# Optimization experiments

Measured on AMD Instinct MI355X. Metric: run time of the kernel, lower is better.

The kernel has to match this reference:

```python
import jax, jax.numpy as jnp
import numpy as np

D, P, R, F = 512, 64, 32, 256  # directions, points per ray, rank, virtual subcarriers


def setup_inputs() -> dict:
    key = jax.random.key(0)
    ks = jax.random.split(key, 6)
    return {
        "att_re": jax.random.normal(ks[0], (D, P, R), dtype=jnp.float32),
        "att_im": jax.random.normal(ks[1], (D, P, R), dtype=jnp.float32),
        "rad_re": jax.random.normal(ks[2], (D, P, R), dtype=jnp.float32),
        "rad_im": jax.random.normal(ks[3], (D, P, R), dtype=jnp.float32),
        "freq_re": jax.random.normal(ks[4], (F, R), dtype=jnp.float32),
        "freq_im": jax.random.normal(ks[5], (F, R), dtype=jnp.float32),
        "max_ray_length": 200,
    }


def reference(att_re, att_im, rad_re, rad_im, freq_re, freq_im, max_ray_length):
    att = (att_re + 1j * att_im).astype(jnp.complex64)   # (D,P,R)
    rad = (rad_re + 1j * rad_im).astype(jnp.complex64)   # (D,P,R)
    fv = (freq_re + 1j * freq_im).astype(jnp.complex64)  # (F,R)

    num_points = att.shape[1]
    num_dirs = att.shape[0]
    delta_t = jnp.asarray(max_ray_length / num_points, dtype=jnp.float32)

    # prefix-sum of conjugated attenuation along the ray (u_hat_rho)
    u_hat_rho = jnp.cumsum(att.conj() * delta_t, axis=1)  # (D,P,R)

    # Project each rank-R vector onto each frequency basis vector.
    # The original's v_outer / v_outer_outer einsums factor exactly into these dot products.
    a_proj = jnp.einsum('dpr,fr->dpf', att.conj(), fv)        # (D,P,F)
    r_proj = jnp.einsum('dpr,fr->dpf', rad.conj(), fv)        # (D,P,F)
    u_proj = jnp.einsum('dpr,fr->dpf', u_hat_rho.conj(), fv)  # (D,P,F)

    # first-order: sum over all points; second-order: points k >= 1 only
    first = jnp.sum(r_proj * a_proj, axis=(0, 1))                                   # (F,)
    second = jnp.sum(r_proj[:, 1:] * a_proj[:, 1:] * u_proj[:, 1:], axis=(0, 1))    # (F,)

    csi = (first + second) * delta_t / num_dirs  # (F,) complex64
    return csi
```

## Files before the change

kernel.cpp:

```cpp
#include <hip/hip_runtime.h>

#define ND 512
#define NP 64
#define NR 32
#define NF 256
#define RS 40

typedef __attribute__((ext_vector_type(8))) short bf16x8;
typedef __attribute__((ext_vector_type(4))) float f32x4;
typedef __attribute__((ext_vector_type(4))) unsigned int uint4v;

__device__ inline unsigned short f2bf(float x) {
    unsigned u = __builtin_bit_cast(unsigned, x);
    u += 0x7FFFu + ((u >> 16) & 1u);
    return (unsigned short)(u >> 16);
}
__device__ inline unsigned pack2(float a, float b) {
    return (unsigned)f2bf(a) | ((unsigned)f2bf(b) << 16);
}
__device__ inline bf16x8 neg8(bf16x8 v) {
    uint4v u = __builtin_bit_cast(uint4v, v);
    u ^= (uint4v){0x80008000u, 0x80008000u, 0x80008000u, 0x80008000u};
    return __builtin_bit_cast(bf16x8, u);
}

__global__ __launch_bounds__(256) void lrrt_bprep_kernel(
    const float* __restrict__ fre, const float* __restrict__ fim,
    unsigned short* __restrict__ ws)
{
    const int tid = blockIdx.x * 256 + threadIdx.x;
    const int plane = tid >> 11;
    const int i4 = (tid & 2047) * 4;
    const float* src = plane ? fim : fre;
    const float4 x = *(const float4*)(src + i4);
    *(uint2*)(ws + plane * (NF * NR) + i4) = make_uint2(pack2(x.x, x.y), pack2(x.z, x.w));
}

__global__ __launch_bounds__(256, 4) void lrrt_main_kernel(
    const float* __restrict__ att_re, const float* __restrict__ att_im,
    const float* __restrict__ rad_re, const float* __restrict__ rad_im,
    const unsigned short* __restrict__ wsB, const int* __restrict__ mrl,
    float* __restrict__ out)
{
    __shared__ __align__(16) unsigned short s_a[6][NP * RS];
    __shared__ float s_tot[256];
    __shared__ float s_red[4][128][2];

    const int t = threadIdx.x;
    const int h = blockIdx.x & 1;
    const int d = blockIdx.x >> 1;
    const size_t base = (size_t)d * (NP * NR);
    const int lane = t & 63, wv = t >> 6, kg = lane >> 4, m_lo = lane & 15;
    const float dt = (float)(*mrl) / (float)NP;

#pragma unroll
    for (int half = 0; half < 2; ++half) {
        const int w = t + half * 256;
        const int p = w >> 3;
        const int c = (w & 7) * 4;
        const size_t g = base + (size_t)p * NR + c;
        const int lo = p * RS + c;
        float4 x;
        x = *(const float4*)(att_re + g);
        *(uint2*)&s_a[0][lo] = make_uint2(pack2(x.x, x.y), pack2(x.z, x.w));
        x = *(const float4*)(att_im + g);
        *(uint2*)&s_a[1][lo] = make_uint2(pack2(x.x, x.y), pack2(x.z, x.w));
        x = *(const float4*)(rad_re + g);
        *(uint2*)&s_a[2][lo] = make_uint2(pack2(x.x, x.y), pack2(x.z, x.w));
        x = *(const float4*)(rad_im + g);
        *(uint2*)&s_a[3][lo] = make_uint2(pack2(x.x, x.y), pack2(x.z, x.w));
    }

    const int cs_r = t & 31, cs_reim = (t >> 5) & 1, cs_seg = t >> 6;
    float vals[16];
    {
        const float* src = cs_reim ? att_im : att_re;
        float run = 0.f;
#pragma unroll
        for (int i = 0; i < 16; ++i) {
            run += src[base + (size_t)(cs_seg * 16 + i) * NR + cs_r];
            vals[i] = run;
        }
        s_tot[t] = run;
    }
    __syncthreads();

    {
        float off = 0.f;
#pragma unroll
        for (int s = 0; s < 3; ++s)
            if (s < cs_seg) off += s_tot[s * 64 + cs_reim * 32 + cs_r];
        const float sc = cs_reim ? -dt : dt;
        unsigned short* dst = s_a[4 + cs_reim];
#pragma unroll
        for (int i = 0; i < 16; ++i) {
            const int p = cs_seg * 16 + i;
            dst[p * RS + cs_r] = (p == 0) ? (unsigned short)0
                                          : f2bf(sc * (vals[i] + off));
        }
    }
    __syncthreads();

    const int aoff = (wv * 16 + m_lo) * RS + 8 * kg;
    const bf16x8 a_r = *(const bf16x8*)&s_a[0][aoff];
    const bf16x8 a_i = *(const bf16x8*)&s_a[1][aoff];
    const bf16x8 r_r = *(const bf16x8*)&s_a[2][aoff];
    const bf16x8 r_i = *(const bf16x8*)&s_a[3][aoff];
    const bf16x8 c_r = *(const bf16x8*)&s_a[4][aoff];
    const bf16x8 c_i = *(const bf16x8*)&s_a[5][aoff];

    const f32x4 zero = {0.f, 0.f, 0.f, 0.f};

#pragma unroll 1
    for (int q = 0; q < 8; ++q) {
        const int f = 16 * (8 * h + q) + m_lo;
        const size_t boff = (size_t)f * NR + 8 * kg;
        const bf16x8 vr = *(const bf16x8*)(wsB + boff);
        const bf16x8 vi = *(const bf16x8*)(wsB + NF * NR + boff);
        const bf16x8 vn = neg8(vr);

        f32x4 Are = __builtin_amdgcn_mfma_f32_16x16x32_bf16(a_r, vr, zero, 0, 0, 0);
        f32x4 Aim = __builtin_amdgcn_mfma_f32_16x16x32_bf16(a_r, vi, zero, 0, 0, 0);
        f32x4 Bre = __builtin_amdgcn_mfma_f32_16x16x32_bf16(r_r, vr, zero, 0, 0, 0);
        f32x4 Bim = __builtin_amdgcn_mfma_f32_16x16x32_bf16(r_r, vi, zero, 0, 0, 0);
        f32x4 Ure = __builtin_amdgcn_mfma_f32_16x16x32_bf16(c_r, vr, zero, 0, 0, 0);
        f32x4 Uim = __builtin_amdgcn_mfma_f32_16x16x32_bf16(c_r, vi, zero, 0, 0, 0);
        Are = __builtin_amdgcn_mfma_f32_16x16x32_bf16(a_i, vi, Are, 0, 0, 0);
        Aim = __builtin_amdgcn_mfma_f32_16x16x32_bf16(a_i, vn, Aim, 0, 0, 0);
        Bre = __builtin_amdgcn_mfma_f32_16x16x32_bf16(r_i, vi, Bre, 0, 0, 0);
        Bim = __builtin_amdgcn_mfma_f32_16x16x32_bf16(r_i, vn, Bim, 0, 0, 0);
        Ure = __builtin_amdgcn_mfma_f32_16x16x32_bf16(c_i, vi, Ure, 0, 0, 0);
        Uim = __builtin_amdgcn_mfma_f32_16x16x32_bf16(c_i, vn, Uim, 0, 0, 0);

        float sr = 0.f, si = 0.f;
#pragma unroll
        for (int i = 0; i < 4; ++i) {
            const float qre = Bre[i] * Are[i] - Bim[i] * Aim[i];
            const float qim = Bre[i] * Aim[i] + Bim[i] * Are[i];
            const float cre = 1.0f + Ure[i];
            const float cim = Uim[i];
            sr = fmaf(qre, cre, fmaf(-qim, cim, sr));
            si = fmaf(qim, cre, fmaf(qre, cim, si));
        }
        sr += __shfl_xor(sr, 16, 64); si += __shfl_xor(si, 16, 64);
        sr += __shfl_xor(sr, 32, 64); si += __shfl_xor(si, 32, 64);
        if (lane < 16) {
            s_red[wv][16 * q + lane][0] = sr;
            s_red[wv][16 * q + lane][1] = si;
        }
    }
    __syncthreads();

    const float scale = dt / (float)ND;
    {
        const int lf = t >> 1, comp = t & 1;
        const float v = s_red[0][lf][comp] + s_red[1][lf][comp]
                      + s_red[2][lf][comp] + s_red[3][lf][comp];
        atomicAdd(&out[comp * NF + h * 128 + lf], v * scale);
    }
}

extern "C" void kernel_launch(void* const* d_in, const int* in_sizes, int n_in,
                              void* d_out, int out_size, void* d_ws, size_t ws_size,
                              hipStream_t stream) {
    const float* att_re = (const float*)d_in[0];
    const float* att_im = (const float*)d_in[1];
    const float* rad_re = (const float*)d_in[2];
    const float* rad_im = (const float*)d_in[3];
    const float* freq_re = (const float*)d_in[4];
    const float* freq_im = (const float*)d_in[5];
    const int* mrl = (const int*)d_in[6];
    float* out = (float*)d_out;
    unsigned short* ws = (unsigned short*)d_ws;

    hipMemsetAsync(d_out, 0, (size_t)out_size * sizeof(float), stream);

    lrrt_bprep_kernel<<<16, 256, 0, stream>>>(freq_re, freq_im, ws);
    lrrt_main_kernel<<<2 * ND, 256, 0, stream>>>(
        att_re, att_im, rad_re, rad_im, ws, mrl, out);
}
```

Measured before the change: 96.74 us.

## Move attenuation prefix-sum into prep kernel and load MFMA operands directly from global

The cumulative sum of attenuation along each ray is now computed once in the prep kernel and stored as bf16 in workspace. Previously both halves of each direction repeated it in the main kernel. The main kernel drops its shared-memory staging and both block barriers, loading and converting its MFMA A operands straight from global memory into registers. The cost is an extra workspace round trip and a serial 64-step scan per thread in the prep kernel, which has only 128 blocks and may be latency bound.

```diff
diff --git a/kernel.cpp b/kernel.cpp
--- a/kernel.cpp
+++ b/kernel.cpp
@@ -4,7 +4,10 @@
 #define NP 64
 #define NR 32
 #define NF 256
-#define RS 40
+
+#define PLANE (ND * NP * NR)
+#define B0 (2 * PLANE)
+#define B1 (2 * PLANE + NF * NR)
 
 typedef __attribute__((ext_vector_type(8))) short bf16x8;
 typedef __attribute__((ext_vector_type(4))) float f32x4;
@@ -18,105 +21,87 @@
 __device__ inline unsigned pack2(float a, float b) {
     return (unsigned)f2bf(a) | ((unsigned)f2bf(b) << 16);
 }
+__device__ inline bf16x8 cvt8(float4 a, float4 b) {
+    uint4v u = {pack2(a.x, a.y), pack2(a.z, a.w), pack2(b.x, b.y), pack2(b.z, b.w)};
+    return __builtin_bit_cast(bf16x8, u);
+}
 __device__ inline bf16x8 neg8(bf16x8 v) {
     uint4v u = __builtin_bit_cast(uint4v, v);
     u ^= (uint4v){0x80008000u, 0x80008000u, 0x80008000u, 0x80008000u};
     return __builtin_bit_cast(bf16x8, u);
 }
 
-__global__ __launch_bounds__(256) void lrrt_bprep_kernel(
+__global__ __launch_bounds__(256) void lrrt_prep_kernel(
+    const float* __restrict__ att_re, const float* __restrict__ att_im,
     const float* __restrict__ fre, const float* __restrict__ fim,
-    unsigned short* __restrict__ ws)
+    const int* __restrict__ mrl, unsigned short* __restrict__ ws)
 {
-    const int tid = blockIdx.x * 256 + threadIdx.x;
-    const int plane = tid >> 11;
-    const int i4 = (tid & 2047) * 4;
-    const float* src = plane ? fim : fre;
-    const float4 x = *(const float4*)(src + i4);
-    *(uint2*)(ws + plane * (NF * NR) + i4) = make_uint2(pack2(x.x, x.y), pack2(x.z, x.w));
+    const int t = threadIdx.x;
+    const int bid = blockIdx.x;
+    if (bid < 128) {
+        const int tid = bid * 256 + t;
+        const int d = tid >> 6;
+        const int reim = (tid >> 5) & 1;
+        const int r = tid & 31;
+        const float dt = (float)(*mrl) / (float)NP;
+        const float sc = reim ? -dt : dt;
+        const float* src = reim ? att_im : att_re;
+        const size_t base = (size_t)d * (NP * NR);
+        unsigned short* dst = ws + (size_t)reim * PLANE + base;
+        float run = src[base + r];
+        dst[r] = 0;
+#pragma unroll
+        for (int p = 1; p < NP; ++p) {
+            run += src[base + (size_t)p * NR + r];
+            dst[(size_t)p * NR + r] = f2bf(sc * run);
+        }
+    } else {
+        const int plane = bid - 128;
+        const float* src = plane ? fim : fre;
+        unsigned short* dst = ws + B0 + plane * (NF * NR);
+        for (int k = t; k < (NF * NR) / 4; k += 256) {
+            const float4 x = *(const float4*)(src + (size_t)k * 4);
+            *(uint2*)(dst + (size_t)k * 4) =
+                make_uint2(pack2(x.x, x.y), pack2(x.z, x.w));
+        }
+    }
 }
 
 __global__ __launch_bounds__(256, 4) void lrrt_main_kernel(
     const float* __restrict__ att_re, const float* __restrict__ att_im,
     const float* __restrict__ rad_re, const float* __restrict__ rad_im,
-    const unsigned short* __restrict__ wsB, const int* __restrict__ mrl,
+    const unsigned short* __restrict__ ws, const int* __restrict__ mrl,
     float* __restrict__ out)
 {
-    __shared__ __align__(16) unsigned short s_a[6][NP * RS];
-    __shared__ float s_tot[256];
     __shared__ float s_red[4][128][2];
 
     const int t = threadIdx.x;
     const int h = blockIdx.x & 1;
     const int d = blockIdx.x >> 1;
-    const size_t base = (size_t)d * (NP * NR);
     const int lane = t & 63, wv = t >> 6, kg = lane >> 4, m_lo = lane & 15;
+    const int p = wv * 16 + m_lo;
+    const size_t arow = (size_t)d * (NP * NR) + (size_t)p * NR + 8 * kg;
+
+    const bf16x8 a_r = cvt8(*(const float4*)(att_re + arow),
+                            *(const float4*)(att_re + arow + 4));
+    const bf16x8 a_i = cvt8(*(const float4*)(att_im + arow),
+                            *(const float4*)(att_im + arow + 4));
+    const bf16x8 r_r = cvt8(*(const float4*)(rad_re + arow),
+                            *(const float4*)(rad_re + arow + 4));
+    const bf16x8 r_i = cvt8(*(const float4*)(rad_im + arow),
+                            *(const float4*)(rad_im + arow + 4));
+    const bf16x8 c_r = *(const bf16x8*)(ws + arow);
+    const bf16x8 c_i = *(const bf16x8*)(ws + PLANE + arow);
+
     const float dt = (float)(*mrl) / (float)NP;
-
-#pragma unroll
-    for (int half = 0; half < 2; ++half) {
-        const int w = t + half * 256;
-        const int p = w >> 3;
-        const int c = (w & 7) * 4;
-        const size_t g = base + (size_t)p * NR + c;
-        const int lo = p * RS + c;
-        float4 x;
-        x = *(const float4*)(att_re + g);
-        *(uint2*)&s_a[0][lo] = make_uint2(pack2(x.x, x.y), pack2(x.z, x.w));
-        x = *(const float4*)(att_im + g);
-        *(uint2*)&s_a[1][lo] = make_uint2(pack2(x.x, x.y), pack2(x.z, x.w));
-        x = *(const float4*)(rad_re + g);
-        *(uint2*)&s_a[2][lo] = make_uint2(pack2(x.x, x.y), pack2(x.z, x.w));
-        x = *(const float4*)(rad_im + g);
-        *(uint2*)&s_a[3][lo] = make_uint2(pack2(x.x, x.y), pack2(x.z, x.w));
-    }
-
-    const int cs_r = t & 31, cs_reim = (t >> 5) & 1, cs_seg = t >> 6;
-    float vals[16];
-    {
-        const float* src = cs_reim ? att_im : att_re;
-        float run = 0.f;
-#pragma unroll
-        for (int i = 0; i < 16; ++i) {
-            run += src[base + (size_t)(cs_seg * 16 + i) * NR + cs_r];
-            vals[i] = run;
-        }
-        s_tot[t] = run;
-    }
-    __syncthreads();
-
-    {
-        float off = 0.f;
-#pragma unroll
-        for (int s = 0; s < 3; ++s)
-            if (s < cs_seg) off += s_tot[s * 64 + cs_reim * 32 + cs_r];
-        const float sc = cs_reim ? -dt : dt;
-        unsigned short* dst = s_a[4 + cs_reim];
-#pragma unroll
-        for (int i = 0; i < 16; ++i) {
-            const int p = cs_seg * 16 + i;
-            dst[p * RS + cs_r] = (p == 0) ? (unsigned short)0
-                                          : f2bf(sc * (vals[i] + off));
-        }
-    }
-    __syncthreads();
-
-    const int aoff = (wv * 16 + m_lo) * RS + 8 * kg;
-    const bf16x8 a_r = *(const bf16x8*)&s_a[0][aoff];
-    const bf16x8 a_i = *(const bf16x8*)&s_a[1][aoff];
-    const bf16x8 r_r = *(const bf16x8*)&s_a[2][aoff];
-    const bf16x8 r_i = *(const bf16x8*)&s_a[3][aoff];
-    const bf16x8 c_r = *(const bf16x8*)&s_a[4][aoff];
-    const bf16x8 c_i = *(const bf16x8*)&s_a[5][aoff];
-
     const f32x4 zero = {0.f, 0.f, 0.f, 0.f};
 
 #pragma unroll 1
     for (int q = 0; q < 8; ++q) {
         const int f = 16 * (8 * h + q) + m_lo;
         const size_t boff = (size_t)f * NR + 8 * kg;
-        const bf16x8 vr = *(const bf16x8*)(wsB + boff);
-        const bf16x8 vi = *(const bf16x8*)(wsB + NF * NR + boff);
+        const bf16x8 vr = *(const bf16x8*)(ws + B0 + boff);
+        const bf16x8 vi = *(const bf16x8*)(ws + B1 + boff);
         const bf16x8 vn = neg8(vr);
 
         f32x4 Are = __builtin_amdgcn_mfma_f32_16x16x32_bf16(a_r, vr, zero, 0, 0, 0);
@@ -175,7 +160,7 @@
 
     hipMemsetAsync(d_out, 0, (size_t)out_size * sizeof(float), stream);
 
-    lrrt_bprep_kernel<<<16, 256, 0, stream>>>(freq_re, freq_im, ws);
+    lrrt_prep_kernel<<<130, 256, 0, stream>>>(att_re, att_im, freq_re, freq_im, mrl, ws);
     lrrt_main_kernel<<<2 * ND, 256, 0, stream>>>(
         att_re, att_im, rad_re, rad_im, ws, mrl, out);
 }
```

Result: slower. 101.1 us (+4.5%).

## Fuse frequency-basis bf16 prep into main kernel and process all frequencies per block

Applied to the files above, without the earlier changes.

Removes the separate bf16 conversion kernel for the frequency basis; each block now loads fp32 freq vectors directly, converts them in registers and software-prefetches the next tile. Each block handles one direction across all 256 frequencies instead of splitting frequencies over two blocks, which halves redundant loading and cumsum of att/rad data. The final atomic adds are rotated per direction to spread contention across output addresses. In exchange, each block does redundant fp32 loads and conversions of the frequency table, and the grid has half as many blocks.

```diff
diff --git a/kernel.cpp b/kernel.cpp
--- a/kernel.cpp
+++ b/kernel.cpp
@@ -1,4 +1,6 @@
 #include <hip/hip_runtime.h>
+#include <hip/hip_bf16.h>
+#include <string.h>
 
 #define ND 512
 #define NP 64
@@ -10,13 +12,23 @@
 typedef __attribute__((ext_vector_type(4))) float f32x4;
 typedef __attribute__((ext_vector_type(4))) unsigned int uint4v;
 
+__device__ inline unsigned pk(float x, float y) {
+    __hip_bfloat162 h = __float22bfloat162_rn(make_float2(x, y));
+    unsigned u;
+    memcpy(&u, &h, sizeof(u));
+    return u;
+}
+__device__ inline uint2 pk4(float4 x) {
+    return make_uint2(pk(x.x, x.y), pk(x.z, x.w));
+}
+__device__ inline bf16x8 cvt8(float4 a, float4 b) {
+    uint4v u = {pk(a.x, a.y), pk(a.z, a.w), pk(b.x, b.y), pk(b.z, b.w)};
+    return __builtin_bit_cast(bf16x8, u);
+}
 __device__ inline unsigned short f2bf(float x) {
     unsigned u = __builtin_bit_cast(unsigned, x);
     u += 0x7FFFu + ((u >> 16) & 1u);
     return (unsigned short)(u >> 16);
-}
-__device__ inline unsigned pack2(float a, float b) {
-    return (unsigned)f2bf(a) | ((unsigned)f2bf(b) << 16);
 }
 __device__ inline bf16x8 neg8(bf16x8 v) {
     uint4v u = __builtin_bit_cast(uint4v, v);
@@ -24,31 +36,18 @@
     return __builtin_bit_cast(bf16x8, u);
 }
 
-__global__ __launch_bounds__(256) void lrrt_bprep_kernel(
-    const float* __restrict__ fre, const float* __restrict__ fim,
-    unsigned short* __restrict__ ws)
-{
-    const int tid = blockIdx.x * 256 + threadIdx.x;
-    const int plane = tid >> 11;
-    const int i4 = (tid & 2047) * 4;
-    const float* src = plane ? fim : fre;
-    const float4 x = *(const float4*)(src + i4);
-    *(uint2*)(ws + plane * (NF * NR) + i4) = make_uint2(pack2(x.x, x.y), pack2(x.z, x.w));
-}
-
-__global__ __launch_bounds__(256, 4) void lrrt_main_kernel(
+__global__ __launch_bounds__(256, 4) void lrrt_mono_kernel(
     const float* __restrict__ att_re, const float* __restrict__ att_im,
     const float* __restrict__ rad_re, const float* __restrict__ rad_im,
-    const unsigned short* __restrict__ wsB, const int* __restrict__ mrl,
-    float* __restrict__ out)
+    const float* __restrict__ freq_re, const float* __restrict__ freq_im,
+    const int* __restrict__ mrl, float* __restrict__ out)
 {
     __shared__ __align__(16) unsigned short s_a[6][NP * RS];
     __shared__ float s_tot[256];
-    __shared__ float s_red[4][128][2];
+    __shared__ float s_red[4][NF][2];
 
     const int t = threadIdx.x;
-    const int h = blockIdx.x & 1;
-    const int d = blockIdx.x >> 1;
+    const int d = blockIdx.x;
     const size_t base = (size_t)d * (NP * NR);
     const int lane = t & 63, wv = t >> 6, kg = lane >> 4, m_lo = lane & 15;
     const float dt = (float)(*mrl) / (float)NP;
@@ -60,15 +59,10 @@
         const int c = (w & 7) * 4;
         const size_t g = base + (size_t)p * NR + c;
         const int lo = p * RS + c;
-        float4 x;
-        x = *(const float4*)(att_re + g);
-        *(uint2*)&s_a[0][lo] = make_uint2(pack2(x.x, x.y), pack2(x.z, x.w));
-        x = *(const float4*)(att_im + g);
-        *(uint2*)&s_a[1][lo] = make_uint2(pack2(x.x, x.y), pack2(x.z, x.w));
-        x = *(const float4*)(rad_re + g);
-        *(uint2*)&s_a[2][lo] = make_uint2(pack2(x.x, x.y), pack2(x.z, x.w));
-        x = *(const float4*)(rad_im + g);
-        *(uint2*)&s_a[3][lo] = make_uint2(pack2(x.x, x.y), pack2(x.z, x.w));
+        *(uint2*)&s_a[0][lo] = pk4(*(const float4*)(att_re + g));
+        *(uint2*)&s_a[1][lo] = pk4(*(const float4*)(att_im + g));
+        *(uint2*)&s_a[2][lo] = pk4(*(const float4*)(rad_re + g));
+        *(uint2*)&s_a[3][lo] = pk4(*(const float4*)(rad_im + g));
     }
 
     const int cs_r = t & 31, cs_reim = (t >> 5) & 1, cs_seg = t >> 6;
@@ -111,12 +105,23 @@
 
     const f32x4 zero = {0.f, 0.f, 0.f, 0.f};
 
+    const size_t boff0 = (size_t)m_lo * NR + 8 * kg;
+    float4 br0 = *(const float4*)(freq_re + boff0);
+    float4 br1 = *(const float4*)(freq_re + boff0 + 4);
+    float4 bi0 = *(const float4*)(freq_im + boff0);
+    float4 bi1 = *(const float4*)(freq_im + boff0 + 4);
+
 #pragma unroll 1
-    for (int q = 0; q < 8; ++q) {
-        const int f = 16 * (8 * h + q) + m_lo;
-        const size_t boff = (size_t)f * NR + 8 * kg;
-        const bf16x8 vr = *(const bf16x8*)(wsB + boff);
-        const bf16x8 vi = *(const bf16x8*)(wsB + NF * NR + boff);
+    for (int q = 0; q < 16; ++q) {
+        const bf16x8 vr = cvt8(br0, br1);
+        const bf16x8 vi = cvt8(bi0, bi1);
+        if (q < 15) {
+            const size_t bo = (size_t)(16 * (q + 1) + m_lo) * NR + 8 * kg;
+            br0 = *(const float4*)(freq_re + bo);
+            br1 = *(const float4*)(freq_re + bo + 4);
+            bi0 = *(const float4*)(freq_im + bo);
+            bi1 = *(const float4*)(freq_im + bo + 4);
+        }
         const bf16x8 vn = neg8(vr);
 
         f32x4 Are = __builtin_amdgcn_mfma_f32_16x16x32_bf16(a_r, vr, zero, 0, 0, 0);
@@ -152,11 +157,13 @@
     __syncthreads();
 
     const float scale = dt / (float)ND;
-    {
-        const int lf = t >> 1, comp = t & 1;
-        const float v = s_red[0][lf][comp] + s_red[1][lf][comp]
-                      + s_red[2][lf][comp] + s_red[3][lf][comp];
-        atomicAdd(&out[comp * NF + h * 128 + lf], v * scale);
+#pragma unroll
+    for (int j = 0; j < 2; ++j) {
+        const int o = ((t + 256 * j) + 2 * d) & 511;
+        const int f = o & 255, comp = o >> 8;
+        const float v = s_red[0][f][comp] + s_red[1][f][comp]
+                      + s_red[2][f][comp] + s_red[3][f][comp];
+        atomicAdd(&out[o], v * scale);
     }
 }
 
@@ -171,11 +178,9 @@
     const float* freq_im = (const float*)d_in[5];
     const int* mrl = (const int*)d_in[6];
     float* out = (float*)d_out;
-    unsigned short* ws = (unsigned short*)d_ws;
 
-    hipMemsetAsync(d_out, 0, (size_t)out_size * sizeof(float), stream);
+    (void)hipMemsetAsync(d_out, 0, (size_t)out_size * sizeof(float), stream);
 
-    lrrt_bprep_kernel<<<16, 256, 0, stream>>>(freq_re, freq_im, ws);
-    lrrt_main_kernel<<<2 * ND, 256, 0, stream>>>(
-        att_re, att_im, rad_re, rad_im, ws, mrl, out);
+    lrrt_mono_kernel<<<ND, 256, 0, stream>>>(
+        att_re, att_im, rad_re, rad_im, freq_re, freq_im, mrl, out);
 }
```

After: 102.6 us. +6.0%, slower.
